# Optimization experiments

Measured on AMD Instinct MI355X. Metric: run time of the kernel, lower is better.

The kernel has to match this reference:

```python
import jax, jax.numpy as jnp
import numpy as np

NUM_EXPERTS = 16
TOPK = 2
IN_DIM = 1024
OUT_DIM = 1024
LAMBDA_AUX = 1.0


def setup_inputs() -> dict:
    key = jax.random.key(0)
    ks = jax.random.split(key, 5)
    scale_in = 1.0 / np.sqrt(IN_DIM)
    x = jax.random.normal(ks[0], (8192, IN_DIM), dtype=jnp.float32)
    # gating Linear(input_dim, num_experts): weight [E, Din], bias [E]
    Wg = jax.random.uniform(ks[1], (NUM_EXPERTS, IN_DIM), jnp.float32, -scale_in, scale_in)
    bg = jax.random.uniform(ks[2], (NUM_EXPERTS,), jnp.float32, -scale_in, scale_in)
    # experts: Linear(input_dim, output_dim) each -> stacked [E, Dout, Din], [E, Dout]
    We = jax.random.uniform(ks[3], (NUM_EXPERTS, OUT_DIM, IN_DIM), jnp.float32, -scale_in, scale_in)
    be = jax.random.uniform(ks[4], (NUM_EXPERTS, OUT_DIM), jnp.float32, -scale_in, scale_in)
    return {"x": x, "Wg": Wg, "bg": bg, "We": We, "be": be}


def _moe_forward(x, Wg, bg, We, be):
    # gating logits [B, E]
    gate_logits = x @ Wg.T + bg
    top_k_values, top_k_indices = jax.lax.top_k(gate_logits, TOPK)  # [B, k]
    # softmax over logits with non-topk masked to -inf == softmax over topk values
    top_k_probs = jax.nn.softmax(top_k_values, axis=-1)  # [B, k]
    # compute every expert's output for every token, then gather the topk
    all_out = jnp.einsum('bd,eod->beo', x, We) + be  # [B, E, Dout]
    sel = jnp.take_along_axis(all_out, top_k_indices[:, :, None], axis=1)  # [B, k, Dout]
    output = jnp.sum(sel * top_k_probs[:, :, None], axis=1)  # [B, Dout]
    # aux load-balancing loss: CV of per-expert summed gate probs (zeros off-topk)
    expert_load = jnp.zeros((NUM_EXPERTS,), dtype=gate_logits.dtype).at[
        top_k_indices.reshape(-1)].add(top_k_probs.reshape(-1))
    load_mean = jnp.mean(expert_load)
    load_std = jnp.std(expert_load, ddof=1)  # torch std is unbiased
    aux_loss = load_std / load_mean
    return output, LAMBDA_AUX * aux_loss


def reference(x, Wg, bg, We, be):
    return _moe_forward(x, Wg, bg, We, be)
```

## Files before the change

### kernel.cpp

```cpp
#include <hip/hip_runtime.h>
#include <hip/hip_bf16.h>

#define NUM_EXPERTS 16
#define IN_DIM 1024
#define OUT_DIM 1024
#define BTOK 8192
#define NSLOT (2 * BTOK)
#define MCAP 320
#define MAX_DESC 80
#define NGATE 1024

typedef __attribute__((ext_vector_type(4))) float f32x4;
typedef __attribute__((ext_vector_type(4))) int   i32x4;
typedef __attribute__((ext_vector_type(4))) unsigned short u16x4;
typedef __attribute__((ext_vector_type(8))) short short8;
typedef __attribute__((ext_vector_type(8))) __bf16 bf16x8;


static __device__ inline unsigned short f2bf(float f) {
    union { float f; unsigned u; } v; v.f = f;
    unsigned u = v.u;
    unsigned r = (u + 0x7FFFu + ((u >> 16) & 1u)) >> 16;
    return (unsigned short)r;
}

static __device__ inline float bf2f(unsigned short b) {
    union { unsigned u; float f; } v; v.u = ((unsigned)b) << 16;
    return v.f;
}

static __device__ inline short8 pack8(float4 a, float4 b) {
    short8 s;
    s[0] = (short)f2bf(a.x); s[1] = (short)f2bf(a.y);
    s[2] = (short)f2bf(a.z); s[3] = (short)f2bf(a.w);
    s[4] = (short)f2bf(b.x); s[5] = (short)f2bf(b.y);
    s[6] = (short)f2bf(b.z); s[7] = (short)f2bf(b.w);
    return s;
}

static __device__ inline bf16x8 ldfrag(const unsigned short* p) {
    i32x4 v = *(const i32x4*)p;
    return __builtin_bit_cast(bf16x8, v);
}

#define GLOAD_LDS16(g, l)                                                     \
    __builtin_amdgcn_global_load_lds(                                         \
        (const __attribute__((address_space(1))) void*)(g),                   \
        (__attribute__((address_space(3))) void*)(l), 16, 0, 0)

__global__ __launch_bounds__(256) void convert_we(
    const float* __restrict__ We, unsigned short* __restrict__ Web)
{
    size_t i = ((size_t)blockIdx.x * 256 + threadIdx.x) * 8;
    const float4* s = (const float4*)(We + i);
    float4 v0 = s[0], v1 = s[1];
    *(short8*)(Web + i) = pack8(v0, v1);
}

__global__ __launch_bounds__(256) void gate_kernel(
    const float* __restrict__ x, const float* __restrict__ Wg,
    const float* __restrict__ bg,
    int* __restrict__ eidx, float* __restrict__ prob,
    float* __restrict__ partialLoad, int* __restrict__ partialCount,
    unsigned short* __restrict__ xb)
{
    __shared__ float sLoad[NUM_EXPERTS];
    __shared__ int   sCnt[NUM_EXPERTS];

    int tid = threadIdx.x, lane = tid & 63, wave = tid >> 6;
    if (tid < NUM_EXPERTS) { sLoad[tid] = 0.f; sCnt[tid] = 0; }
    __syncthreads();

    const bool wb = (xb != nullptr);
    int tbase = blockIdx.x * 8 + wave * 2;

    const float4* xr0 = (const float4*)(x + (size_t)(tbase + 0) * IN_DIM);
    const float4* xr1 = (const float4*)(x + (size_t)(tbase + 1) * IN_DIM);

    float4 xv0[4], xv1[4];
    #pragma unroll
    for (int pass = 0; pass < 4; ++pass) {
        xv0[pass] = xr0[pass * 64 + lane];
        xv1[pass] = xr1[pass * 64 + lane];
    }
    if (wb) {
        #pragma unroll
        for (int pass = 0; pass < 4; ++pass) {
            u16x4 b0, b1;
            b0[0]=f2bf(xv0[pass].x); b0[1]=f2bf(xv0[pass].y);
            b0[2]=f2bf(xv0[pass].z); b0[3]=f2bf(xv0[pass].w);
            b1[0]=f2bf(xv1[pass].x); b1[1]=f2bf(xv1[pass].y);
            b1[2]=f2bf(xv1[pass].z); b1[3]=f2bf(xv1[pass].w);
            size_t c = (size_t)(pass * 64 + lane) * 4;
            *(u16x4*)(xb + (size_t)(tbase + 0) * IN_DIM + c) = b0;
            *(u16x4*)(xb + (size_t)(tbase + 1) * IN_DIM + c) = b1;
        }
    }

    float acc0[NUM_EXPERTS], acc1[NUM_EXPERTS];
    #pragma unroll
    for (int e = 0; e < NUM_EXPERTS; ++e) { acc0[e] = 0.f; acc1[e] = 0.f; }

    #pragma unroll
    for (int pass = 0; pass < 4; ++pass) {
        int kb = pass * 256 + lane * 4;
        #pragma unroll
        for (int e = 0; e < NUM_EXPERTS; ++e) {
            float4 wv = *(const float4*)(Wg + e * IN_DIM + kb);
            acc0[e] += xv0[pass].x*wv.x + xv0[pass].y*wv.y
                     + xv0[pass].z*wv.z + xv0[pass].w*wv.w;
            acc1[e] += xv1[pass].x*wv.x + xv1[pass].y*wv.y
                     + xv1[pass].z*wv.z + xv1[pass].w*wv.w;
        }
    }

    #pragma unroll
    for (int e = 0; e < NUM_EXPERTS; ++e) {
        float v0 = acc0[e], v1 = acc1[e];
        #pragma unroll
        for (int off = 32; off; off >>= 1) {
            v0 += __shfl_xor(v0, off);
            v1 += __shfl_xor(v1, off);
        }
        acc0[e] = v0; acc1[e] = v1;
    }

    if (lane == 0) {
        #pragma unroll
        for (int j = 0; j < 2; ++j) {
            int t = tbase + j;
            float v0 = -1e30f, v1 = -1e30f; int i0 = 0, i1 = 0;
            #pragma unroll
            for (int e = 0; e < NUM_EXPERTS; ++e) {
                float a = (j == 0) ? acc0[e] : acc1[e];
                float v = a + bg[e];
                if (v > v0) { v1 = v0; i1 = i0; v0 = v; i0 = e; }
                else if (v > v1) { v1 = v; i1 = e; }
            }
            float t1 = expf(v1 - v0);
            float inv = 1.f / (1.f + t1);
            float p0 = inv, p1 = t1 * inv;
            eidx[2 * t]     = i0;  eidx[2 * t + 1] = i1;
            prob[2 * t]     = p0;  prob[2 * t + 1] = p1;
            atomicAdd(&sCnt[i0], 1);
            atomicAdd(&sCnt[i1], 1);
            atomicAdd(&sLoad[i0], p0);
            atomicAdd(&sLoad[i1], p1);
        }
    }
    __syncthreads();
    if (tid < NUM_EXPERTS) {
        partialLoad[blockIdx.x * NUM_EXPERTS + tid]  = sLoad[tid];
        partialCount[blockIdx.x * NUM_EXPERTS + tid] = sCnt[tid];
    }
}

__global__ __launch_bounds__(256) void finalize_gate(
    int* __restrict__ offsets, int* __restrict__ cursor,
    const float* __restrict__ partialLoad, const int* __restrict__ partialCount,
    float* __restrict__ aux_out, int* __restrict__ descs)
{
    __shared__ float sL[256];
    __shared__ int   sC[256];
    int tid = threadIdx.x;
    int e = tid & 15, part = tid >> 4;
    float s = 0.f; int c = 0;
    #pragma unroll 8
    for (int b = 0; b < 64; ++b) {
        int blk = part * 64 + b;
        s += partialLoad[blk * NUM_EXPERTS + e];
        c += partialCount[blk * NUM_EXPERTS + e];
    }
    sL[tid] = s; sC[tid] = c;
    __syncthreads();
    if (tid < NUM_EXPERTS) {
        float sum = 0.f; int cc = 0;
        #pragma unroll
        for (int p = 0; p < 16; ++p) { sum += sL[p * 16 + tid]; cc += sC[p * 16 + tid]; }
        sL[tid] = sum; sC[tid] = cc;
    }
    __syncthreads();
    if (tid == 0) {
        int off = 0, n = 0;
        for (int e2 = 0; e2 < NUM_EXPERTS; ++e2) {
            offsets[e2] = off; cursor[e2] = off;
            int ne = sC[e2];
            int ntm = (ne + MCAP - 1) / MCAP;
            if (ne > 0 && ne <= 4 * MCAP) ntm = 4;
            for (int tm = 0; tm < ntm; ++tm) descs[1 + n++] = (e2 << 8) | tm;
            off += ne;
        }
        offsets[NUM_EXPERTS] = off;
        descs[0] = n;
        float mean = 0.f;
        for (int e2 = 0; e2 < NUM_EXPERTS; ++e2) mean += sL[e2];
        mean *= (1.f / NUM_EXPERTS);
        float var = 0.f;
        for (int e2 = 0; e2 < NUM_EXPERTS; ++e2) {
            float d = sL[e2] - mean; var += d * d;
        }
        var *= (1.f / (NUM_EXPERTS - 1));
        aux_out[0] = sqrtf(var) / mean;
    }
}

__global__ __launch_bounds__(256) void scatter_kernel(
    const int* __restrict__ eidx, int* __restrict__ cursor,
    int* __restrict__ perm)
{
    __shared__ int lc[NUM_EXPERTS];
    __shared__ int lbase[NUM_EXPERTS];
    int tid = threadIdx.x;
    if (tid < NUM_EXPERTS) lc[tid] = 0;
    __syncthreads();
    int t = blockIdx.x * 256 + tid;
    int e0 = eidx[2 * t], e1 = eidx[2 * t + 1];
    int lp0 = atomicAdd(&lc[e0], 1);
    int lp1 = atomicAdd(&lc[e1], 1);
    __syncthreads();
    if (tid < NUM_EXPERTS) lbase[tid] = atomicAdd(&cursor[tid], lc[tid]);
    __syncthreads();
    perm[lbase[e0] + lp0] = 2 * t;
    perm[lbase[e1] + lp1] = 2 * t + 1;
}

__global__ __launch_bounds__(512, 1) void expert_gemm_bf16(
    const unsigned short* __restrict__ xb, const unsigned short* __restrict__ Web,
    const int* __restrict__ perm, const int* __restrict__ offsets,
    const int* __restrict__ descs, unsigned short* __restrict__ y2)
{
    int bid = blockIdx.x;
    int xcd = bid & 7, j = bid >> 3;
    int d  = xcd + 8 * (j >> 2);
    int tn = j & 3;
    if (d >= descs[0]) return;
    int de = descs[1 + d];
    int e = de >> 8, tm = de & 255;
    int g0 = offsets[e], g1 = offsets[e + 1];

    __shared__ unsigned short As[2][MCAP * 64];
    __shared__ unsigned short Bs[2][256 * 64];

    int tid = threadIdx.x, lane = tid & 63, w = tid >> 6;
    int wm = w >> 2, wn = w & 3;

    const char* aPtr[5];
    const char* bPtr[4];
    #pragma unroll
    for (int i = 0; i < 5; ++i) {
        int c = i * 512 + tid;
        int row = c >> 3, ss = c & 7;
        int s = ss ^ (row & 7);
        int gIdx = g0 + tm * MCAP + row;
        if (gIdx > NSLOT - 1) gIdx = NSLOT - 1;
        int tok = perm[gIdx] >> 1;
        aPtr[i] = (const char*)(xb + (size_t)tok * IN_DIM + s * 8);
    }
    #pragma unroll
    for (int i = 0; i < 4; ++i) {
        int c = i * 512 + tid;
        int row = c >> 3, ss = c & 7;
        int s = ss ^ (row & 7);
        bPtr[i] = (const char*)(Web + ((size_t)e * OUT_DIM + tn * 256 + row) * IN_DIM + s * 8);
    }

    f32x4 acc[10][4];
    #pragma unroll
    for (int m = 0; m < 10; ++m)
        #pragma unroll
        for (int n = 0; n < 4; ++n) {
            acc[m][n][0] = 0.f; acc[m][n][1] = 0.f;
            acc[m][n][2] = 0.f; acc[m][n][3] = 0.f;
        }

    #pragma unroll
    for (int i = 0; i < 5; ++i)
        GLOAD_LDS16(aPtr[i], &As[0][(i * 512 + w * 64) * 8]);
    #pragma unroll
    for (int i = 0; i < 4; ++i)
        GLOAD_LDS16(bPtr[i], &Bs[0][(i * 512 + w * 64) * 8]);

    for (int t = 0; t < IN_DIM / 64; ++t) {
        int cur = t & 1;
        if (t < IN_DIM / 64 - 1) {
            int kByte = (t + 1) * 128;
            #pragma unroll
            for (int i = 0; i < 5; ++i)
                GLOAD_LDS16(aPtr[i] + kByte, &As[cur ^ 1][(i * 512 + w * 64) * 8]);
            #pragma unroll
            for (int i = 0; i < 4; ++i)
                GLOAD_LDS16(bPtr[i] + kByte, &Bs[cur ^ 1][(i * 512 + w * 64) * 8]);
            asm volatile("s_waitcnt vmcnt(9)" ::: "memory");
        } else {
            asm volatile("s_waitcnt vmcnt(0)" ::: "memory");
        }
        __builtin_amdgcn_sched_barrier(0);
        __builtin_amdgcn_s_barrier();
        __builtin_amdgcn_sched_barrier(0);

        __builtin_amdgcn_s_setprio(1);
        #pragma unroll
        for (int ks = 0; ks < 2; ++ks) {
            bf16x8 aF[10], bF[4];
            #pragma unroll
            for (int m = 0; m < 10; ++m) {
                int row = wm * 160 + m * 16 + (lane & 15);
                int chunk = (ks * 4 + (lane >> 4)) ^ (row & 7);
                aF[m] = ldfrag(&As[cur][row * 64 + chunk * 8]);
            }
            #pragma unroll
            for (int n = 0; n < 4; ++n) {
                int row = wn * 64 + n * 16 + (lane & 15);
                int chunk = (ks * 4 + (lane >> 4)) ^ (row & 7);
                bF[n] = ldfrag(&Bs[cur][row * 64 + chunk * 8]);
            }
            #pragma unroll
            for (int m = 0; m < 10; ++m)
                #pragma unroll
                for (int n = 0; n < 4; ++n)
                    acc[m][n] = __builtin_amdgcn_mfma_f32_16x16x32_bf16(
                        aF[m], bF[n], acc[m][n], 0, 0, 0);
        }
        __builtin_amdgcn_s_setprio(0);

        asm volatile("s_waitcnt lgkmcnt(0)" ::: "memory");
        __builtin_amdgcn_sched_barrier(0);
        __builtin_amdgcn_s_barrier();
        __builtin_amdgcn_sched_barrier(0);
    }

    #pragma unroll
    for (int m = 0; m < 10; ++m)
        #pragma unroll
        for (int r = 0; r < 4; ++r) {
            int row = wm * 160 + m * 16 + (lane >> 4) * 4 + r;
            int gIdx = g0 + tm * MCAP + row;
            if (gIdx < g1) {
                int ent = perm[gIdx];
                size_t base = (size_t)ent * OUT_DIM + tn * 256 + wn * 64 + (lane & 15);
                #pragma unroll
                for (int n = 0; n < 4; ++n)
                    y2[base + n * 16] = f2bf(acc[m][n][r]);
            }
        }
}

__global__ __launch_bounds__(256) void combine_kernel(
    float* __restrict__ out, const int* __restrict__ eidx,
    const float* __restrict__ prob, const float* __restrict__ be)
{
    int t   = blockIdx.x;
    int tid = threadIdx.x;
    int e0 = eidx[2 * t], e1 = eidx[2 * t + 1];
    float p0 = prob[2 * t], p1 = prob[2 * t + 1];

    const unsigned short* y = (const unsigned short*)out;
    u16x4 a = *(const u16x4*)(y + (size_t)(2 * t)     * OUT_DIM + tid * 4);
    u16x4 b = *(const u16x4*)(y + (size_t)(2 * t + 1) * OUT_DIM + tid * 4);
    float4 b0 = *(const float4*)(be + e0 * OUT_DIM + tid * 4);
    float4 b1 = *(const float4*)(be + e1 * OUT_DIM + tid * 4);

    float4 r;
    r.x = p0 * (bf2f(a[0]) + b0.x) + p1 * (bf2f(b[0]) + b1.x);
    r.y = p0 * (bf2f(a[1]) + b0.y) + p1 * (bf2f(b[1]) + b1.y);
    r.z = p0 * (bf2f(a[2]) + b0.z) + p1 * (bf2f(b[2]) + b1.z);
    r.w = p0 * (bf2f(a[3]) + b0.w) + p1 * (bf2f(b[3]) + b1.w);

    __syncthreads();
    *(float4*)(out + (size_t)t * OUT_DIM + tid * 4) = r;
}

__global__ __launch_bounds__(256) void expert_gemm_f32(
    const float* __restrict__ x, const float* __restrict__ We,
    const float* __restrict__ be,
    const int* __restrict__ perm, const float* __restrict__ prob,
    const int* __restrict__ offsets, float* __restrict__ out)
{
    int e  = blockIdx.z;
    int g0 = offsets[e], g1 = offsets[e + 1];
    int ne = g1 - g0;
    int tm = blockIdx.y;
    if (tm * 128 >= ne) return;
    int tn = blockIdx.x;

    __shared__ unsigned short As[128 * 64];
    __shared__ unsigned short Bs[128 * 64];

    int tid  = threadIdx.x;
    int lane = tid & 63;
    int wave = tid >> 6;
    int wm = wave >> 1, wn = wave & 1;

    const float* aSrc[4]; bool aValid[4];
    #pragma unroll
    for (int i = 0; i < 4; ++i) {
        int c = tid + 256 * i;
        int row = c >> 3;
        int gIdx = g0 + tm * 128 + row;
        if (gIdx < g1) {
            int tok = perm[gIdx] >> 1;
            aSrc[i] = x + (size_t)tok * IN_DIM;
            aValid[i] = true;
        } else { aSrc[i] = x; aValid[i] = false; }
    }
    const float* bSrcBase = We + (size_t)e * OUT_DIM * IN_DIM;

    f32x4 acc[4][4];
    #pragma unroll
    for (int m = 0; m < 4; ++m)
        #pragma unroll
        for (int n = 0; n < 4; ++n) {
            acc[m][n][0] = 0.f; acc[m][n][1] = 0.f;
            acc[m][n][2] = 0.f; acc[m][n][3] = 0.f;
        }

    for (int k0 = 0; k0 < IN_DIM; k0 += 64) {
        __syncthreads();
        #pragma unroll
        for (int i = 0; i < 4; ++i) {
            int c = tid + 256 * i;
            int row = c >> 3, s = c & 7;
            float4 v0, v1;
            if (aValid[i]) {
                const float* p = aSrc[i] + k0 + s * 8;
                v0 = *(const float4*)p;
                v1 = *(const float4*)(p + 4);
            } else {
                v0 = make_float4(0.f, 0.f, 0.f, 0.f); v1 = v0;
            }
            int ss = s ^ (row & 7);
            *(short8*)&As[row * 64 + ss * 8] = pack8(v0, v1);
        }
        #pragma unroll
        for (int i = 0; i < 4; ++i) {
            int c = tid + 256 * i;
            int row = c >> 3, s = c & 7;
            int o = tn * 128 + row;
            const float* p = bSrcBase + (size_t)o * IN_DIM + k0 + s * 8;
            float4 v0 = *(const float4*)p;
            float4 v1 = *(const float4*)(p + 4);
            int ss = s ^ (row & 7);
            *(short8*)&Bs[row * 64 + ss * 8] = pack8(v0, v1);
        }
        __syncthreads();

        #pragma unroll
        for (int ks = 0; ks < 2; ++ks) {
            bf16x8 aF[4], bF[4];
            #pragma unroll
            for (int m = 0; m < 4; ++m) {
                int row = wm * 64 + m * 16 + (lane & 15);
                int chunk = (ks * 4 + (lane >> 4)) ^ (row & 7);
                aF[m] = ldfrag(&As[row * 64 + chunk * 8]);
            }
            #pragma unroll
            for (int n = 0; n < 4; ++n) {
                int row = wn * 64 + n * 16 + (lane & 15);
                int chunk = (ks * 4 + (lane >> 4)) ^ (row & 7);
                bF[n] = ldfrag(&Bs[row * 64 + chunk * 8]);
            }
            #pragma unroll
            for (int m = 0; m < 4; ++m)
                #pragma unroll
                for (int n = 0; n < 4; ++n)
                    acc[m][n] = __builtin_amdgcn_mfma_f32_16x16x32_bf16(
                        aF[m], bF[n], acc[m][n], 0, 0, 0);
        }
    }

    int   rowTok[4][4];
    float rowP[4][4];
    bool  rowV[4][4];
    #pragma unroll
    for (int m = 0; m < 4; ++m)
        #pragma unroll
        for (int r = 0; r < 4; ++r) {
            int row = wm * 64 + m * 16 + (lane >> 4) * 4 + r;
            int gIdx = g0 + tm * 128 + row;
            if (gIdx < g1) {
                int entry = perm[gIdx];
                rowTok[m][r] = entry >> 1;
                rowP[m][r]   = prob[entry];
                rowV[m][r]   = true;
            } else rowV[m][r] = false;
        }
    #pragma unroll
    for (int n = 0; n < 4; ++n) {
        int col = tn * 128 + wn * 64 + n * 16 + (lane & 15);
        float bias = be[e * OUT_DIM + col];
        #pragma unroll
        for (int m = 0; m < 4; ++m)
            #pragma unroll
            for (int r = 0; r < 4; ++r)
                if (rowV[m][r]) {
                    float v = acc[m][n][r] + bias;
                    atomicAdd(&out[(size_t)rowTok[m][r] * OUT_DIM + col],
                              rowP[m][r] * v);
                }
    }
}

extern "C" void kernel_launch(void* const* d_in, const int* in_sizes, int n_in,
                              void* d_out, int out_size, void* d_ws, size_t ws_size,
                              hipStream_t stream) {
    const float* x  = (const float*)d_in[0];
    const float* Wg = (const float*)d_in[1];
    const float* bg = (const float*)d_in[2];
    const float* We = (const float*)d_in[3];
    const float* be = (const float*)d_in[4];
    float* out = (float*)d_out;

    const size_t WEB_BYTES = (size_t)NUM_EXPERTS * OUT_DIM * IN_DIM * 2;
    const size_t XB_BYTES  = (size_t)BTOK * IN_DIM * 2;
    const size_t MISC      = (size_t)NSLOT * 12 + (size_t)NGATE * NUM_EXPERTS * 8 + 8192;
    bool full = ws_size >= WEB_BYTES + XB_BYTES + MISC;

    char* w = (char*)d_ws;
    unsigned short* Web = nullptr;
    unsigned short* xb  = nullptr;
    if (full) {
        Web = (unsigned short*)w; w += WEB_BYTES;
        xb  = (unsigned short*)w; w += XB_BYTES;
    }
    int*   offsets     = (int*)w;    w += 128;
    int*   cursor      = (int*)w;    w += 64;
    int*   descs       = (int*)w;    w += (1 + MAX_DESC) * 4 + 60;
    int*   eidx        = (int*)w;    w += (size_t)NSLOT * 4;
    float* probArr     = (float*)w;  w += (size_t)NSLOT * 4;
    int*   perm        = (int*)w;    w += (size_t)NSLOT * 4;
    float* partialLoad = (float*)w;  w += (size_t)NGATE * NUM_EXPERTS * 4;
    int*   partialCnt  = (int*)w;    w += (size_t)NGATE * NUM_EXPERTS * 4;

    if (!full)
        hipMemsetAsync(d_out, 0, (size_t)out_size * sizeof(float), stream);

    if (full)
        convert_we<<<NUM_EXPERTS * OUT_DIM * IN_DIM / (256 * 8), 256, 0, stream>>>(We, Web);

    gate_kernel<<<NGATE, 256, 0, stream>>>(x, Wg, bg, eidx, probArr,
                                           partialLoad, partialCnt,
                                           full ? xb : nullptr);
    finalize_gate<<<1, 256, 0, stream>>>(offsets, cursor, partialLoad, partialCnt,
                                         out + (size_t)BTOK * OUT_DIM, descs);
    scatter_kernel<<<BTOK / 256, 256, 0, stream>>>(eidx, cursor, perm);

    if (full) {
        expert_gemm_bf16<<<MAX_DESC * 4, 512, 0, stream>>>(
            xb, Web, perm, offsets, descs, (unsigned short*)d_out);
        combine_kernel<<<BTOK, 256, 0, stream>>>(out, eidx, probArr, be);
    } else {
        dim3 grid(OUT_DIM / 128, NSLOT / 128, NUM_EXPERTS);
        expert_gemm_f32<<<grid, 256, 0, stream>>>(x, We, be, perm, probArr,
                                                  offsets, out);
    }
}
```

Measured before the change: 113.3 us.

## Fuse expert weight bf16 conversion into gating kernel via interleaved blocks

Removes the separate convert_we launch and folds the We fp32-to-bf16 conversion into the gating kernel. Every third block converts a 32K-element chunk of We with nontemporal loads and stores, and the other blocks do gating on remapped token indices. The aim is to overlap the bandwidth-bound weight conversion with the gating work and drop one launch. The gating blocks and conversion blocks now share CUs, and each conversion block does 16 iterations of work.

```diff
diff --git a/kernel.cpp b/kernel.cpp
--- a/kernel.cpp
+++ b/kernel.cpp
@@ -9,6 +9,7 @@
 #define MCAP 320
 #define MAX_DESC 80
 #define NGATE 1024
+#define NCONV 512
 
 typedef __attribute__((ext_vector_type(4))) float f32x4;
 typedef __attribute__((ext_vector_type(4))) int   i32x4;
@@ -38,6 +39,15 @@
     return s;
 }
 
+static __device__ inline short8 pack8v(f32x4 a, f32x4 b) {
+    short8 s;
+    s[0] = (short)f2bf(a[0]); s[1] = (short)f2bf(a[1]);
+    s[2] = (short)f2bf(a[2]); s[3] = (short)f2bf(a[3]);
+    s[4] = (short)f2bf(b[0]); s[5] = (short)f2bf(b[1]);
+    s[6] = (short)f2bf(b[2]); s[7] = (short)f2bf(b[3]);
+    return s;
+}
+
 static __device__ inline bf16x8 ldfrag(const unsigned short* p) {
     i32x4 v = *(const i32x4*)p;
     return __builtin_bit_cast(bf16x8, v);
@@ -48,31 +58,42 @@
         (const __attribute__((address_space(1))) void*)(g),                   \
         (__attribute__((address_space(3))) void*)(l), 16, 0, 0)
 
-__global__ __launch_bounds__(256) void convert_we(
-    const float* __restrict__ We, unsigned short* __restrict__ Web)
-{
-    size_t i = ((size_t)blockIdx.x * 256 + threadIdx.x) * 8;
-    const float4* s = (const float4*)(We + i);
-    float4 v0 = s[0], v1 = s[1];
-    *(short8*)(Web + i) = pack8(v0, v1);
-}
-
-__global__ __launch_bounds__(256) void gate_kernel(
+__global__ __launch_bounds__(256) void gate_conv_kernel(
     const float* __restrict__ x, const float* __restrict__ Wg,
     const float* __restrict__ bg,
     int* __restrict__ eidx, float* __restrict__ prob,
     float* __restrict__ partialLoad, int* __restrict__ partialCount,
-    unsigned short* __restrict__ xb)
+    unsigned short* __restrict__ xb,
+    const float* __restrict__ We, unsigned short* __restrict__ Web)
 {
     __shared__ float sLoad[NUM_EXPERTS];
     __shared__ int   sCnt[NUM_EXPERTS];
 
+    int bid = blockIdx.x;
+    int r3  = bid % 3;
     int tid = threadIdx.x, lane = tid & 63, wave = tid >> 6;
+
+    if (r3 == 2) {
+        if (Web != nullptr) {
+            int cb = bid / 3;
+            #pragma unroll 4
+            for (int i = 0; i < 16; ++i) {
+                size_t off = (((size_t)cb * 16 + i) * 256 + tid) * 8;
+                f32x4 v0 = __builtin_nontemporal_load((const f32x4*)(We + off));
+                f32x4 v1 = __builtin_nontemporal_load((const f32x4*)(We + off + 4));
+                __builtin_nontemporal_store(pack8v(v0, v1), (short8*)(Web + off));
+            }
+        }
+        return;
+    }
+
+    int gb = (bid / 3) * 2 + r3;
+
     if (tid < NUM_EXPERTS) { sLoad[tid] = 0.f; sCnt[tid] = 0; }
     __syncthreads();
 
     const bool wb = (xb != nullptr);
-    int tbase = blockIdx.x * 8 + wave * 2;
+    int tbase = gb * 8 + wave * 2;
 
     const float4* xr0 = (const float4*)(x + (size_t)(tbase + 0) * IN_DIM);
     const float4* xr1 = (const float4*)(x + (size_t)(tbase + 1) * IN_DIM);
@@ -150,8 +171,8 @@
     }
     __syncthreads();
     if (tid < NUM_EXPERTS) {
-        partialLoad[blockIdx.x * NUM_EXPERTS + tid]  = sLoad[tid];
-        partialCount[blockIdx.x * NUM_EXPERTS + tid] = sCnt[tid];
+        partialLoad[gb * NUM_EXPERTS + tid]  = sLoad[tid];
+        partialCount[gb * NUM_EXPERTS + tid] = sCnt[tid];
     }
 }
 
@@ -534,12 +555,9 @@
     if (!full)
         hipMemsetAsync(d_out, 0, (size_t)out_size * sizeof(float), stream);
 
-    if (full)
-        convert_we<<<NUM_EXPERTS * OUT_DIM * IN_DIM / (256 * 8), 256, 0, stream>>>(We, Web);
-
-    gate_kernel<<<NGATE, 256, 0, stream>>>(x, Wg, bg, eidx, probArr,
-                                           partialLoad, partialCnt,
-                                           full ? xb : nullptr);
+    gate_conv_kernel<<<NGATE + NCONV, 256, 0, stream>>>(
+        x, Wg, bg, eidx, probArr, partialLoad, partialCnt,
+        full ? xb : nullptr, We, full ? Web : nullptr);
     finalize_gate<<<1, 256, 0, stream>>>(offsets, cursor, partialLoad, partialCnt,
                                          out + (size_t)BTOK * OUT_DIM, descs);
     scatter_kernel<<<BTOK / 256, 256, 0, stream>>>(eidx, cursor, perm);
```

After: 122.8 us. +8.3%, slower.
